# Kernel optimization log

Hardware: AMD Instinct MI355X
Metric: run time of the kernel (lower is better)

Reference implementation:

```python
import jax, jax.numpy as jnp
import numpy as np

COMMITMENT_COST = 0.25


def setup_inputs() -> dict:
    key = jax.random.key(0)
    k1, k2 = jax.random.split(key)
    inputs = jax.random.normal(k1, (64, 1024, 128), dtype=jnp.float32)
    # torch.rand init -> uniform [0, 1)
    codewords = jax.random.uniform(k2, (1024, 128), dtype=jnp.float32)
    return {"inputs": inputs, "codewords": codewords}


def reference(inputs, codewords):
    sg = jax.lax.stop_gradient
    D = codewords.shape[-1]
    flat = inputs.reshape(-1, D)  # (N, D)
    distances = (
        jnp.sum(flat * flat, axis=1, keepdims=True)
        - 2.0 * flat @ codewords.T
        + jnp.sum(codewords * codewords, axis=1)
    )  # (N, K)
    encoding_indices = jnp.argmin(distances, axis=1)  # (N,)
    quantized = codewords[encoding_indices].reshape(inputs.shape)

    quantizing_loss = jnp.mean((sg(quantized) - inputs) ** 2)
    commitment_loss = jnp.mean((quantized - sg(inputs)) ** 2)
    loss = quantizing_loss + COMMITMENT_COST * commitment_loss

    # straight-through estimator
    quantized = inputs + sg(quantized - inputs)
    return quantized, encoding_indices[:, None], loss
```

## Files before the change

### kernel.cpp

```cpp
#include <hip/hip_runtime.h>
#include <stdint.h>


typedef short     bf16x8 __attribute__((ext_vector_type(8)));
typedef float     f32x4  __attribute__((ext_vector_type(4)));
typedef unsigned short u16x8 __attribute__((ext_vector_type(8)));
typedef unsigned short u16x2 __attribute__((ext_vector_type(2)));

constexpr int N_ROWS = 65536;
constexpr int K_CODES = 1024;
constexpr int D = 128;
constexpr float MARGIN = 0.01f;

__device__ __forceinline__ unsigned short f32_to_bf16_rn(float f) {
    unsigned u = __float_as_uint(f);
    unsigned r = (u + 0x7FFFu + ((u >> 16) & 1u)) >> 16;
    return (unsigned short)r;
}
__device__ __forceinline__ float bf16_to_f32(unsigned short h) {
    return __uint_as_float(((unsigned)h) << 16);
}

__device__ __forceinline__ void gload_lds16(const void* g, void* l) {
    __builtin_amdgcn_global_load_lds(
        (const __attribute__((address_space(1))) unsigned int*)g,
        (__attribute__((address_space(3))) unsigned int*)l, 16, 0, 0);
}

__global__ __launch_bounds__(64) void vq_prep_cw(const float* __restrict__ cw,
                                                 unsigned short* __restrict__ Cp,
                                                 float* __restrict__ cnorm,
                                                 int* __restrict__ rcnt,
                                                 double* __restrict__ acc) {
    const int k = blockIdx.x;
    const int lane = threadIdx.x;
    float2 v = reinterpret_cast<const float2*>(cw + (size_t)k * D)[lane];
    float s = v.x * v.x + v.y * v.y;
#pragma unroll
    for (int off = 32; off; off >>= 1) s += __shfl_down(s, off, 64);
    if (lane == 0) cnorm[k] = s;
    if (lane == 0 && k == 0) { *rcnt = 0; *acc = 0.0; }

    unsigned short hx = f32_to_bf16_rn(v.x), hy = f32_to_bf16_rn(v.y);
    unsigned short lx = f32_to_bf16_rn(v.x - bf16_to_f32(hx));
    unsigned short ly = f32_to_bf16_rn(v.y - bf16_to_f32(hy));
    size_t off0 = (size_t)k * D + lane * 2;
    u16x2 hv; hv[0] = hx; hv[1] = hy;
    u16x2 lv; lv[0] = lx; lv[1] = ly;
    *reinterpret_cast<u16x2*>(Cp + off0) = hv;
    *reinterpret_cast<u16x2*>(Cp + 131072 + off0) = lv;
}

__global__ __launch_bounds__(256, 3) void vq_argmin_mfma(
    const float* __restrict__ x,
    const unsigned short* __restrict__ Cp,
    const float* __restrict__ cnorm,
    float* __restrict__ half_bv,
    float* __restrict__ half_bv2,
    int* __restrict__ half_bi,
    float* __restrict__ xnorm) {
    __shared__ unsigned char Bs[3][2][8192];

    const int tid = threadIdx.x;
    const int wave = tid >> 6;
    const int lane = tid & 63;
    const int l15 = lane & 15;
    const int lg = lane >> 4;
    const int tile = blockIdx.x >> 1;
    const int khalf = blockIdx.x & 1;
    const int wrow = tile * 128 + wave * 32;

    const char* Cpb = reinterpret_cast<const char*>(Cp);
    auto stageB = [&](int c, int b) {
#pragma unroll
        for (int u = 0; u < 4; ++u) {
            int t = wave * 4 + u;
            int pl = t >> 3;
            int cwl = (t & 7) * 4 + lg;
            int q = l15 * 16;
            const char* src = Cpb + pl * 262144 + khalf * 131072
                              + ((size_t)(c * 32 + cwl)) * 256 + (q ^ ((cwl & 7) << 4));
            void* dst = (void*)&Bs[b][pl][(t & 7) * 1024];
            gload_lds16(src, dst);
        }
    };
    stageB(0, 0);

    bf16x8 A[2][4][2];
    float xn[2] = {0.f, 0.f};
#pragma unroll
    for (int r2 = 0; r2 < 2; ++r2) {
        const float* xr0 = x + (size_t)(wrow + r2 * 16 + l15) * D;
#pragma unroll
        for (int s = 0; s < 4; ++s) {
            const float4* xf = reinterpret_cast<const float4*>(xr0 + s * 32 + lg * 8);
            float4 f0 = xf[0];
            float4 f1 = xf[1];
            float in[8] = {f0.x, f0.y, f0.z, f0.w, f1.x, f1.y, f1.z, f1.w};
            u16x8 hv, lv;
#pragma unroll
            for (int e = 0; e < 8; ++e) {
                xn[r2] += in[e] * in[e];
                unsigned short h = f32_to_bf16_rn(in[e]);
                hv[e] = h;
                lv[e] = f32_to_bf16_rn(in[e] - bf16_to_f32(h));
            }
            A[r2][s][0] = *reinterpret_cast<bf16x8*>(&hv);
            A[r2][s][1] = *reinterpret_cast<bf16x8*>(&lv);
        }
    }
#pragma unroll
    for (int r2 = 0; r2 < 2; ++r2) {
        xn[r2] += __shfl_xor(xn[r2], 16, 64);
        xn[r2] += __shfl_xor(xn[r2], 32, 64);
        if (khalf == 0 && lg == 0) xnorm[wrow + r2 * 16 + l15] = xn[r2];
    }

    stageB(1, 1);

    float bv[2][4], bv2[2][4];
    int bi_[2][4];
#pragma unroll
    for (int r2 = 0; r2 < 2; ++r2)
#pragma unroll
        for (int i = 0; i < 4; ++i) { bv[r2][i] = 3.4e38f; bv2[r2][i] = 3.4e38f; bi_[r2][i] = 0; }

    const int cb = l15 * 256;
    const int swz = (l15 & 7) << 4;
    int kb[4];
#pragma unroll
    for (int s = 0; s < 4; ++s) kb[s] = (s * 64 + lg * 16) ^ swz;

    auto computeChunk = [&](int c, int buf) {
        f32x4 acc[2][2];
#pragma unroll
        for (int r2 = 0; r2 < 2; ++r2)
#pragma unroll
            for (int j = 0; j < 2; ++j) acc[r2][j] = (f32x4)(0.f);

        __builtin_amdgcn_s_setprio(1);
#pragma unroll
        for (int s = 0; s < 4; ++s) {
            bf16x8 bh[2], bl[2];
#pragma unroll
            for (int j = 0; j < 2; ++j) {
                int ad = j * 4096 + cb + kb[s];
                bh[j] = *reinterpret_cast<const bf16x8*>(&Bs[buf][0][ad]);
                bl[j] = *reinterpret_cast<const bf16x8*>(&Bs[buf][1][ad]);
            }
#pragma unroll
            for (int r2 = 0; r2 < 2; ++r2)
#pragma unroll
                for (int j = 0; j < 2; ++j) {
                    acc[r2][j] = __builtin_amdgcn_mfma_f32_16x16x32_bf16(
                        A[r2][s][0], bh[j], acc[r2][j], 0, 0, 0);
                    acc[r2][j] = __builtin_amdgcn_mfma_f32_16x16x32_bf16(
                        A[r2][s][0], bl[j], acc[r2][j], 0, 0, 0);
                    acc[r2][j] = __builtin_amdgcn_mfma_f32_16x16x32_bf16(
                        A[r2][s][1], bh[j], acc[r2][j], 0, 0, 0);
                }
        }
        __builtin_amdgcn_s_setprio(0);

#pragma unroll
        for (int j = 0; j < 2; ++j) {
            int col = khalf * 512 + c * 32 + j * 16 + l15;
            float cn = cnorm[col];
#pragma unroll
            for (int r2 = 0; r2 < 2; ++r2)
#pragma unroll
                for (int i = 0; i < 4; ++i) {
                    float sc = cn - 2.f * acc[r2][j][i];
                    if (sc < bv[r2][i]) {
                        bv2[r2][i] = bv[r2][i];
                        bv[r2][i] = sc;
                        bi_[r2][i] = col;
                    } else if (sc < bv2[r2][i]) {
                        bv2[r2][i] = sc;
                    }
                }
        }
    };

    int cur = 0;
    for (int c = 0; c < 15; ++c) {
        asm volatile("s_waitcnt vmcnt(4)\n\ts_barrier" ::: "memory");
        if (c < 14) {
            int stg = cur + 2;
            if (stg >= 3) stg -= 3;
            stageB(c + 2, stg);
        }
        computeChunk(c, cur);
        cur = (cur == 2) ? 0 : cur + 1;
    }
    asm volatile("s_waitcnt vmcnt(0)\n\ts_barrier" ::: "memory");
    computeChunk(15, cur);

#pragma unroll
    for (int r2 = 0; r2 < 2; ++r2)
#pragma unroll
        for (int i = 0; i < 4; ++i) {
            float v = bv[r2][i], v2 = bv2[r2][i];
            int ix = bi_[r2][i];
#pragma unroll
            for (int off = 1; off < 16; off <<= 1) {
                float ov = __shfl_xor(v, off, 64);
                float ov2 = __shfl_xor(v2, off, 64);
                int oi = __shfl_xor(ix, off, 64);
                float nv2 = fminf(fminf(v2, ov2), fmaxf(v, ov));
                if (ov < v || (ov == v && oi < ix)) { v = ov; ix = oi; }
                v2 = nv2;
            }
            if (l15 == 0) {
                int row = wrow + r2 * 16 + lg * 4 + i;
                int o = khalf * N_ROWS + row;
                half_bv[o] = v;
                half_bv2[o] = v2;
                half_bi[o] = ix;
            }
        }
}

__global__ __launch_bounds__(256) void vq_merge(const float* __restrict__ cw,
                                                const float* __restrict__ half_bv,
                                                const float* __restrict__ half_bv2,
                                                const int* __restrict__ half_bi,
                                                const float* __restrict__ xnorm,
                                                float* __restrict__ out_idx_f,
                                                float* __restrict__ qout,
                                                float* __restrict__ rowloss,
                                                int* __restrict__ rcnt,
                                                int* __restrict__ rrows,
                                                double* __restrict__ acc) {
    const int t = threadIdx.x;
    const int d4 = t & 31;
    double lsum = 0.0;

    for (int it = 0; it < 32; ++it) {
        int row = blockIdx.x * 256 + it * 8 + (t >> 5);
        float v0 = half_bv[row], v0b = half_bv2[row];
        int i0 = half_bi[row];
        float v1 = half_bv[N_ROWS + row], v1b = half_bv2[N_ROWS + row];
        int i1 = half_bi[N_ROWS + row];

        bool take0 = (v0 < v1) || (v0 == v1 && i0 <= i1);
        float best = take0 ? v0 : v1;
        int bidx = take0 ? i0 : i1;
        float second = take0 ? fminf(v1, v0b) : fminf(v0, v1b);

        float4 q4 = reinterpret_cast<const float4*>(cw)[(size_t)bidx * 32 + d4];
        reinterpret_cast<float4*>(qout)[(size_t)row * 32 + d4] = q4;

        if (d4 == 0) {
            out_idx_f[row] = (float)bidx;
            float rl = xnorm[row] + best;
            rowloss[row] = rl;
            lsum += (double)rl;
            if (second - best < MARGIN) {
                int p = atomicAdd(rcnt, 1);
                rrows[p] = row;
            }
        }
    }
#pragma unroll
    for (int off = 32; off; off >>= 1) lsum += __shfl_down(lsum, off, 64);
    __shared__ double wsum[4];
    if ((t & 63) == 0) wsum[t >> 6] = lsum;
    __syncthreads();
    if (t == 0) atomicAdd(acc, wsum[0] + wsum[1] + wsum[2] + wsum[3]);
}

__global__ __launch_bounds__(256) void vq_repair(const float* __restrict__ x,
                                                 const float* __restrict__ cw,
                                                 const float* __restrict__ cnorm,
                                                 const float* __restrict__ xnorm,
                                                 const int* __restrict__ rcnt,
                                                 const int* __restrict__ rrows,
                                                 float* __restrict__ out_idx_f,
                                                 float* __restrict__ qout,
                                                 float* __restrict__ rowloss,
                                                 double* __restrict__ acc) {
    __shared__ float xs[16][132];
    __shared__ int rowids[16];
    __shared__ float sval[16][16];
    __shared__ int sidx[16][16];
    __shared__ int fidx[16];

    const int t = threadIdx.x;
    const int count = *rcnt;
    const float4* cw4 = reinterpret_cast<const float4*>(cw);
    double dsum = 0.0;

    for (int g = blockIdx.x; g * 16 < count; g += 512) {
        int nrows = min(16, count - g * 16);
        __syncthreads();
        if (t < 16) rowids[t] = rrows[g * 16 + (t < nrows ? t : 0)];
        __syncthreads();
        for (int i = t; i < 512; i += 256) {
            int r = i >> 5, d4 = i & 31;
            *reinterpret_cast<float4*>(&xs[r][d4 * 4]) =
                reinterpret_cast<const float4*>(x)[(size_t)rowids[r] * 32 + d4];
        }
        __syncthreads();

        const int r = t & 15;
        const int qq = t >> 4;
        float bv = 3.4e38f;
        int bi = 0;
#pragma unroll 2
        for (int kt = 0; kt < 8; ++kt) {
            float a[8] = {0.f, 0.f, 0.f, 0.f, 0.f, 0.f, 0.f, 0.f};
            int k0 = qq * 64 + kt * 8;
            for (int d4 = 0; d4 < 32; ++d4) {
                float4 xv = *reinterpret_cast<const float4*>(&xs[r][d4 * 4]);
#pragma unroll
                for (int kk = 0; kk < 8; ++kk) {
                    float4 cv = cw4[(size_t)(k0 + kk) * 32 + d4];
                    a[kk] += xv.x * cv.x + xv.y * cv.y + xv.z * cv.z + xv.w * cv.w;
                }
            }
#pragma unroll
            for (int kk = 0; kk < 8; ++kk) {
                int k = k0 + kk;
                float sc = cnorm[k] - 2.f * a[kk];
                if (sc < bv) { bv = sc; bi = k; }
            }
        }
        sval[r][qq] = bv;
        sidx[r][qq] = bi;
        __syncthreads();
        if (t < 16) {
            float fv = sval[t][0];
            int fi = sidx[t][0];
#pragma unroll
            for (int q2 = 1; q2 < 16; ++q2) {
                float v = sval[t][q2];
                int ii = sidx[t][q2];
                if (v < fv || (v == fv && ii < fi)) { fv = v; fi = ii; }
            }
            fidx[t] = fi;
            if (t < nrows) {
                int row = rowids[t];
                out_idx_f[row] = (float)fi;
                float nrl = xnorm[row] + fv;
                float orl = rowloss[row];
                rowloss[row] = nrl;
                dsum += (double)nrl - (double)orl;
            }
        }
        __syncthreads();
        for (int i = t; i < 512; i += 256) {
            int rr = i >> 5, d4 = i & 31;
            float4 q4 = cw4[(size_t)fidx[rr] * 32 + d4];
            reinterpret_cast<float4*>(qout)[(size_t)rowids[rr] * 32 + d4] = q4;
        }
    }
#pragma unroll
    for (int off = 32; off; off >>= 1) dsum += __shfl_down(dsum, off, 64);
    __shared__ double wsum[4];
    if ((t & 63) == 0) wsum[t >> 6] = dsum;
    __syncthreads();
    if (t == 0) {
        double b = wsum[0] + wsum[1] + wsum[2] + wsum[3];
        if (b != 0.0) atomicAdd(acc, b);
    }
}

__global__ void vq_loss_final(const double* __restrict__ acc,
                              float* __restrict__ out_loss) {
    *out_loss = (float)(*acc * (1.25 / (double)((size_t)N_ROWS * D)));
}

extern "C" void kernel_launch(void* const* d_in, const int* in_sizes, int n_in,
                              void* d_out, int out_size, void* d_ws, size_t ws_size,
                              hipStream_t stream) {
    const float* x = (const float*)d_in[0];
    const float* cw = (const float*)d_in[1];

    float* qout = (float*)d_out;
    float* out_idx_f = qout + (size_t)N_ROWS * D;
    float* out_loss = out_idx_f + N_ROWS;

    char* w = (char*)d_ws;
    unsigned short* Cp = (unsigned short*)w;          w += 524288;
    float* cnorm = (float*)w;                         w += 4096;
    int* rcnt = (int*)w;                              w += 16;
    double* acc = (double*)w;                         w += 240;
    int* rrows = (int*)w;                             w += 262144;
    float* half_bv = (float*)w;                       w += 524288;
    float* half_bv2 = (float*)w;                      w += 524288;
    int* half_bi = (int*)w;                           w += 524288;
    float* xnorm = (float*)w;                         w += 262144;
    float* rowloss = (float*)w;                       w += 262144;

    vq_prep_cw<<<K_CODES, 64, 0, stream>>>(cw, Cp, cnorm, rcnt, acc);
    vq_argmin_mfma<<<(N_ROWS / 128) * 2, 256, 0, stream>>>(
        x, Cp, cnorm, half_bv, half_bv2, half_bi, xnorm);
    vq_merge<<<N_ROWS / 256, 256, 0, stream>>>(
        cw, half_bv, half_bv2, half_bi, xnorm, out_idx_f, qout, rowloss, rcnt, rrows, acc);
    vq_repair<<<512, 256, 0, stream>>>(
        x, cw, cnorm, xnorm, rcnt, rrows, out_idx_f, qout, rowloss, acc);
    vq_loss_final<<<1, 1, 0, stream>>>(acc, out_loss);
}
```

Before: 255.2 us.

## Fuse argmin and merge into one kernel covering all codewords per block

Each block now scans all 1024 codewords for its 128 rows, so the K-split across two blocks and the separate merge kernel go away. The block writes indices, row losses, repair candidates and the gathered quantized rows itself. Staging changes from a triple-buffered 32-code pipeline to a double-buffered 64-code pipeline with full syncthreads, and occupancy drops from 3 to 2 blocks per CU. This removes the half-result round trip through global memory and one launch, but gives fewer, longer blocks and a weaker load/compute overlap.

```diff
diff --git a/kernel.cpp b/kernel.cpp
--- a/kernel.cpp
+++ b/kernel.cpp
@@ -51,36 +51,42 @@
     *reinterpret_cast<u16x2*>(Cp + 131072 + off0) = lv;
 }
 
-__global__ __launch_bounds__(256, 3) void vq_argmin_mfma(
+__global__ __launch_bounds__(256, 2) void vq_argmin_fused(
     const float* __restrict__ x,
     const unsigned short* __restrict__ Cp,
     const float* __restrict__ cnorm,
-    float* __restrict__ half_bv,
-    float* __restrict__ half_bv2,
-    int* __restrict__ half_bi,
-    float* __restrict__ xnorm) {
-    __shared__ unsigned char Bs[3][2][8192];
+    const float* __restrict__ cw,
+    float* __restrict__ out_idx_f,
+    float* __restrict__ qout,
+    float* __restrict__ rowloss,
+    float* __restrict__ xnorm,
+    int* __restrict__ rcnt,
+    int* __restrict__ rrows,
+    double* __restrict__ acc) {
+    __shared__ unsigned char Bs[2][2][16384];
+    __shared__ int idx_s[128];
+    __shared__ float xs_n[128];
+    __shared__ double wsum[4];
 
     const int tid = threadIdx.x;
     const int wave = tid >> 6;
     const int lane = tid & 63;
     const int l15 = lane & 15;
     const int lg = lane >> 4;
-    const int tile = blockIdx.x >> 1;
-    const int khalf = blockIdx.x & 1;
-    const int wrow = tile * 128 + wave * 32;
+    const int base = blockIdx.x * 128;
+    const int wrow = base + wave * 32;
 
     const char* Cpb = reinterpret_cast<const char*>(Cp);
     auto stageB = [&](int c, int b) {
 #pragma unroll
-        for (int u = 0; u < 4; ++u) {
-            int t = wave * 4 + u;
-            int pl = t >> 3;
-            int cwl = (t & 7) * 4 + lg;
+        for (int u = 0; u < 8; ++u) {
+            int t = wave * 8 + u;
+            int pl = t >> 4;
+            int cwl = (t & 15) * 4 + lg;
             int q = l15 * 16;
-            const char* src = Cpb + pl * 262144 + khalf * 131072
-                              + ((size_t)(c * 32 + cwl)) * 256 + (q ^ ((cwl & 7) << 4));
-            void* dst = (void*)&Bs[b][pl][(t & 7) * 1024];
+            const char* src = Cpb + pl * 262144 + ((size_t)(c * 64 + cwl)) * 256
+                              + (q ^ ((cwl & 7) << 4));
+            void* dst = (void*)&Bs[b][pl][(t & 15) * 1024];
             gload_lds16(src, dst);
         }
     };
@@ -113,10 +119,11 @@
     for (int r2 = 0; r2 < 2; ++r2) {
         xn[r2] += __shfl_xor(xn[r2], 16, 64);
         xn[r2] += __shfl_xor(xn[r2], 32, 64);
-        if (khalf == 0 && lg == 0) xnorm[wrow + r2 * 16 + l15] = xn[r2];
-    }
-
-    stageB(1, 1);
+        if (lg == 0) {
+            xs_n[wave * 32 + r2 * 16 + l15] = xn[r2];
+            xnorm[wrow + r2 * 16 + l15] = xn[r2];
+        }
+    }
 
     float bv[2][4], bv2[2][4];
     int bi_[2][4];
@@ -131,19 +138,24 @@
 #pragma unroll
     for (int s = 0; s < 4; ++s) kb[s] = (s * 64 + lg * 16) ^ swz;
 
-    auto computeChunk = [&](int c, int buf) {
-        f32x4 acc[2][2];
+    asm volatile("s_waitcnt vmcnt(0)" ::: "memory");
+    __syncthreads();
+
+    for (int c = 0; c < 16; ++c) {
+        const int buf = c & 1;
+        if (c < 15) stageB(c + 1, buf ^ 1);
+
+        f32x4 accf[2][4];
 #pragma unroll
         for (int r2 = 0; r2 < 2; ++r2)
 #pragma unroll
-            for (int j = 0; j < 2; ++j) acc[r2][j] = (f32x4)(0.f);
-
-        __builtin_amdgcn_s_setprio(1);
+            for (int j = 0; j < 4; ++j) accf[r2][j] = (f32x4)(0.f);
+
 #pragma unroll
         for (int s = 0; s < 4; ++s) {
-            bf16x8 bh[2], bl[2];
-#pragma unroll
-            for (int j = 0; j < 2; ++j) {
+            bf16x8 bh[4], bl[4];
+#pragma unroll
+            for (int j = 0; j < 4; ++j) {
                 int ad = j * 4096 + cb + kb[s];
                 bh[j] = *reinterpret_cast<const bf16x8*>(&Bs[buf][0][ad]);
                 bl[j] = *reinterpret_cast<const bf16x8*>(&Bs[buf][1][ad]);
@@ -151,26 +163,25 @@
 #pragma unroll
             for (int r2 = 0; r2 < 2; ++r2)
 #pragma unroll
-                for (int j = 0; j < 2; ++j) {
-                    acc[r2][j] = __builtin_amdgcn_mfma_f32_16x16x32_bf16(
-                        A[r2][s][0], bh[j], acc[r2][j], 0, 0, 0);
-                    acc[r2][j] = __builtin_amdgcn_mfma_f32_16x16x32_bf16(
-                        A[r2][s][0], bl[j], acc[r2][j], 0, 0, 0);
-                    acc[r2][j] = __builtin_amdgcn_mfma_f32_16x16x32_bf16(
-                        A[r2][s][1], bh[j], acc[r2][j], 0, 0, 0);
+                for (int j = 0; j < 4; ++j) {
+                    accf[r2][j] = __builtin_amdgcn_mfma_f32_16x16x32_bf16(
+                        A[r2][s][0], bh[j], accf[r2][j], 0, 0, 0);
+                    accf[r2][j] = __builtin_amdgcn_mfma_f32_16x16x32_bf16(
+                        A[r2][s][0], bl[j], accf[r2][j], 0, 0, 0);
+                    accf[r2][j] = __builtin_amdgcn_mfma_f32_16x16x32_bf16(
+                        A[r2][s][1], bh[j], accf[r2][j], 0, 0, 0);
                 }
         }
-        __builtin_amdgcn_s_setprio(0);
-
-#pragma unroll
-        for (int j = 0; j < 2; ++j) {
-            int col = khalf * 512 + c * 32 + j * 16 + l15;
+
+#pragma unroll
+        for (int j = 0; j < 4; ++j) {
+            int col = c * 64 + j * 16 + l15;
             float cn = cnorm[col];
 #pragma unroll
             for (int r2 = 0; r2 < 2; ++r2)
 #pragma unroll
                 for (int i = 0; i < 4; ++i) {
-                    float sc = cn - 2.f * acc[r2][j][i];
+                    float sc = cn - 2.f * accf[r2][j][i];
                     if (sc < bv[r2][i]) {
                         bv2[r2][i] = bv[r2][i];
                         bv[r2][i] = sc;
@@ -180,22 +191,11 @@
                     }
                 }
         }
-    };
-
-    int cur = 0;
-    for (int c = 0; c < 15; ++c) {
-        asm volatile("s_waitcnt vmcnt(4)\n\ts_barrier" ::: "memory");
-        if (c < 14) {
-            int stg = cur + 2;
-            if (stg >= 3) stg -= 3;
-            stageB(c + 2, stg);
-        }
-        computeChunk(c, cur);
-        cur = (cur == 2) ? 0 : cur + 1;
-    }
-    asm volatile("s_waitcnt vmcnt(0)\n\ts_barrier" ::: "memory");
-    computeChunk(15, cur);
-
+        asm volatile("s_waitcnt vmcnt(0)" ::: "memory");
+        __syncthreads();
+    }
+
+    double lsum = 0.0;
 #pragma unroll
     for (int r2 = 0; r2 < 2; ++r2)
 #pragma unroll
@@ -212,62 +212,34 @@
                 v2 = nv2;
             }
             if (l15 == 0) {
-                int row = wrow + r2 * 16 + lg * 4 + i;
-                int o = khalf * N_ROWS + row;
-                half_bv[o] = v;
-                half_bv2[o] = v2;
-                half_bi[o] = ix;
-            }
-        }
-}
-
-__global__ __launch_bounds__(256) void vq_merge(const float* __restrict__ cw,
-                                                const float* __restrict__ half_bv,
-                                                const float* __restrict__ half_bv2,
-                                                const int* __restrict__ half_bi,
-                                                const float* __restrict__ xnorm,
-                                                float* __restrict__ out_idx_f,
-                                                float* __restrict__ qout,
-                                                float* __restrict__ rowloss,
-                                                int* __restrict__ rcnt,
-                                                int* __restrict__ rrows,
-                                                double* __restrict__ acc) {
-    const int t = threadIdx.x;
-    const int d4 = t & 31;
-    double lsum = 0.0;
-
-    for (int it = 0; it < 32; ++it) {
-        int row = blockIdx.x * 256 + it * 8 + (t >> 5);
-        float v0 = half_bv[row], v0b = half_bv2[row];
-        int i0 = half_bi[row];
-        float v1 = half_bv[N_ROWS + row], v1b = half_bv2[N_ROWS + row];
-        int i1 = half_bi[N_ROWS + row];
-
-        bool take0 = (v0 < v1) || (v0 == v1 && i0 <= i1);
-        float best = take0 ? v0 : v1;
-        int bidx = take0 ? i0 : i1;
-        float second = take0 ? fminf(v1, v0b) : fminf(v0, v1b);
-
-        float4 q4 = reinterpret_cast<const float4*>(cw)[(size_t)bidx * 32 + d4];
-        reinterpret_cast<float4*>(qout)[(size_t)row * 32 + d4] = q4;
-
-        if (d4 == 0) {
-            out_idx_f[row] = (float)bidx;
-            float rl = xnorm[row] + best;
-            rowloss[row] = rl;
-            lsum += (double)rl;
-            if (second - best < MARGIN) {
-                int p = atomicAdd(rcnt, 1);
-                rrows[p] = row;
-            }
-        }
-    }
+                int rl_loc = wave * 32 + r2 * 16 + lg * 4 + i;
+                int row = base + rl_loc;
+                out_idx_f[row] = (float)ix;
+                idx_s[rl_loc] = ix;
+                float rl = xs_n[rl_loc] + v;
+                rowloss[row] = rl;
+                lsum += (double)rl;
+                if (v2 - v < MARGIN) {
+                    int p = atomicAdd(rcnt, 1);
+                    rrows[p] = row;
+                }
+            }
+        }
+
 #pragma unroll
     for (int off = 32; off; off >>= 1) lsum += __shfl_down(lsum, off, 64);
-    __shared__ double wsum[4];
-    if ((t & 63) == 0) wsum[t >> 6] = lsum;
+    if (lane == 0) wsum[wave] = lsum;
     __syncthreads();
-    if (t == 0) atomicAdd(acc, wsum[0] + wsum[1] + wsum[2] + wsum[3]);
+    if (tid == 0) atomicAdd(acc, wsum[0] + wsum[1] + wsum[2] + wsum[3]);
+
+    const float4* cw4 = reinterpret_cast<const float4*>(cw);
+    float4* q4 = reinterpret_cast<float4*>(qout);
+#pragma unroll
+    for (int it = 0; it < 16; ++it) {
+        int i = it * 256 + tid;
+        int r = i >> 5, d4 = i & 31;
+        q4[(size_t)(base + r) * 32 + d4] = cw4[(size_t)idx_s[r] * 32 + d4];
+    }
 }
 
 __global__ __launch_bounds__(256) void vq_repair(const float* __restrict__ x,
@@ -387,17 +359,12 @@
     int* rcnt = (int*)w;                              w += 16;
     double* acc = (double*)w;                         w += 240;
     int* rrows = (int*)w;                             w += 262144;
-    float* half_bv = (float*)w;                       w += 524288;
-    float* half_bv2 = (float*)w;                      w += 524288;
-    int* half_bi = (int*)w;                           w += 524288;
     float* xnorm = (float*)w;                         w += 262144;
     float* rowloss = (float*)w;                       w += 262144;
 
     vq_prep_cw<<<K_CODES, 64, 0, stream>>>(cw, Cp, cnorm, rcnt, acc);
-    vq_argmin_mfma<<<(N_ROWS / 128) * 2, 256, 0, stream>>>(
-        x, Cp, cnorm, half_bv, half_bv2, half_bi, xnorm);
-    vq_merge<<<N_ROWS / 256, 256, 0, stream>>>(
-        cw, half_bv, half_bv2, half_bi, xnorm, out_idx_f, qout, rowloss, rcnt, rrows, acc);
+    vq_argmin_fused<<<N_ROWS / 128, 256, 0, stream>>>(
+        x, Cp, cnorm, cw, out_idx_f, qout, rowloss, xnorm, rcnt, rrows, acc);
     vq_repair<<<512, 256, 0, stream>>>(
         x, cw, cnorm, xnorm, rcnt, rrows, out_idx_f, qout, rowloss, acc);
     vq_loss_final<<<1, 1, 0, stream>>>(acc, out_loss);
```

New measurement: 225.7 us. -11.6%, faster.
